# Kernel optimization log

Measured on AMD Instinct MI355X. Metric: run time of the kernel, lower is better.

The kernel has to match this reference:

```python
import jax, jax.numpy as jnp
import numpy as np

S, B, H, K = 2048, 64, 8, 12          # seq_len, input_bits, num_heads, bits per RAM neuron
N_POS = 11                             # bits for relative distance in [0, max_seq_len-1]


def setup_inputs() -> dict:
    key = jax.random.key(0)
    k1, k2, k3, k4, k5 = jax.random.split(key, 5)
    tokens = jax.random.randint(k1, (S, B), 0, 2, dtype=jnp.int32)            # bit tokens
    conn_heads = jax.random.randint(k2, (H, K), 0, 2 * B + N_POS, dtype=jnp.int32)
    head_table = jnp.round(jax.random.uniform(k3, (H, 1 << K))).astype(jnp.float32)  # {0,1} RAM cells
    conn_v = jax.random.randint(k4, (B, K), 0, B, dtype=jnp.int32)
    table_v = jnp.round(jax.random.uniform(k5, (B, 1 << K))).astype(jnp.float32)     # {0,1} RAM cells
    return {"tokens": tokens, "conn_heads": conn_heads, "head_table": head_table,
            "conn_v": conn_v, "table_v": table_v}


def reference(tokens, conn_heads, head_table, conn_v, table_v):
    pow2 = (1 << (K - 1 - jnp.arange(K))).astype(jnp.int32)                 # [K] MSB-first
    tok = tokens.astype(jnp.int32)                                           # [S,B]

    # split each head's 12 connections into query / key / relative-position groups
    grp_q = (conn_heads < B).astype(jnp.int32)
    grp_k = ((conn_heads >= B) & (conn_heads < 2 * B)).astype(jnp.int32)
    grp_p = (conn_heads >= 2 * B).astype(jnp.int32)
    cq = jnp.clip(conn_heads, 0, B - 1)
    ck = jnp.clip(conn_heads - B, 0, B - 1)
    cp = jnp.clip(conn_heads - 2 * B, 0, N_POS - 1)

    # additive address decomposition: addr(i,j,h) = addr_q(i,h)+addr_k(j,h)+addr_p(i-j,h)
    addr_q = (tok[:, cq] * (grp_q * pow2)[None]).sum(-1)                     # [S,H]
    addr_k = (tok[:, ck] * (grp_k * pow2)[None]).sum(-1)                     # [S,H]
    ar = jnp.arange(S)
    posb = ((ar[:, None] >> (N_POS - 1 - jnp.arange(N_POS))[None, :]) & 1).astype(jnp.int32)  # [S,N_POS]
    addr_p = (posb[:, cp] * (grp_p * pow2)[None]).sum(-1)                    # [S,H] indexed by rel dist

    rel = jnp.clip(ar[:, None] - ar[None, :], 0)                             # [S,S]
    addr = addr_q[:, None, :] + addr_k[None, :, :] + addr_p[rel]             # [S,S,H]

    # per-head table lookup, sum over heads = vote counts
    votes = head_table[jnp.arange(H)[None, None, :], addr].sum(-1)           # [S,S]
    causal = ar[None, :] <= ar[:, None]
    votes = jnp.where(causal, votes, 0.0)

    # bit-level value projection: one RAM neuron per output bit
    addr_v = (tok[:, conn_v] * pow2[None, None, :]).sum(-1)                  # [S,B]
    values = table_v[jnp.arange(B)[None, :], addr_v]                         # [S,B]

    # TOP_1 aggregation: first key with max vote; zeros if max vote is 0
    max_vote = votes.max(axis=1)                                             # [S]
    best = jnp.argmax(votes, axis=1)                                         # first occurrence, like the loop
    out = jnp.where((max_vote > 0)[:, None], values[best], 0.0)              # [S,B]
    return out
```

## Files before the change

kernel.cpp:

```cpp
#include <hip/hip_runtime.h>


#define SS 2048
#define BB 64
#define HH 8
#define KK 12
#define NPOS 11
#define TBL 4096
#define TBLW (TBL / 32)

typedef unsigned short u16;
typedef unsigned int u32;
typedef unsigned long long u64;

#define SEG_A (SS * HH)
#define SEG_B (HH * TBL)
#define SEG_C (SS * BB)
#define TOTAL (SEG_A + SEG_B + SEG_C)

__global__ __launch_bounds__(256) void precompute_kernel(
    const int* __restrict__ tokens,
    const int* __restrict__ conn_heads,
    const float* __restrict__ head_table,
    const int* __restrict__ conn_v,
    u16* __restrict__ A16, u16* __restrict__ AK16, u16* __restrict__ P16,
    u32* __restrict__ bits, u16* __restrict__ V16)
{
    const int gid = blockIdx.x * 256 + threadIdx.x;
    if (gid < SEG_A) {
        const int s = gid >> 3;
        const int h = gid & 7;
        int aq = 0, ak = 0, ap = 0;
        #pragma unroll
        for (int k = 0; k < KK; ++k) {
            const int c = conn_heads[h * KK + k];
            const int sh = KK - 1 - k;
            const int cq = min(c, BB - 1);
            const int ck = min(max(c - BB, 0), BB - 1);
            const int cp = min(max(c - 2 * BB, 0), NPOS - 1);
            const int tq = tokens[s * BB + cq] & 1;
            const int tk = tokens[s * BB + ck] & 1;
            const int tp = (s >> (NPOS - 1 - cp)) & 1;
            aq |= (c < BB ? tq : 0) << sh;
            ap |= (c >= 2 * BB ? tp : 0) << sh;
            ak |= ((c >= BB) && (c < 2 * BB) ? tk : 0) << sh;
        }
        A16[gid]  = (u16)aq;
        AK16[gid] = (u16)ak;
        P16[gid]  = (u16)ap;
    } else if (gid < SEG_A + SEG_B) {
        const int t = gid - SEG_A;
        const u64 m = __ballot(head_table[t] > 0.5f);
        if ((t & 63) == 0) {
            bits[(t >> 5) + 0] = (u32)m;
            bits[(t >> 5) + 1] = (u32)(m >> 32);
        }
    } else {
        const int t = gid - (SEG_A + SEG_B);
        const int s = t >> 6;
        const int b = t & 63;
        int av = 0;
        #pragma unroll
        for (int k = 0; k < KK; ++k) {
            av |= (tokens[s * BB + conn_v[b * KK + k]] & 1) << (KK - 1 - k);
        }
        V16[t] = (u16)av;
    }
}

__device__ __forceinline__ int votes_packed(const u32* sbits,
                                            const uint4& q, const uint4& kk, const uint4& pp)
{
    int v = 0;
    u32 w, a0, a1;
    w = q.x | kk.x | pp.x;
    a0 = w & 0xFFFFu; a1 = w >> 16;
    v += (sbits[0 * TBLW + (a0 >> 5)] >> (a0 & 31)) & 1;
    v += (sbits[1 * TBLW + (a1 >> 5)] >> (a1 & 31)) & 1;
    w = q.y | kk.y | pp.y;
    a0 = w & 0xFFFFu; a1 = w >> 16;
    v += (sbits[2 * TBLW + (a0 >> 5)] >> (a0 & 31)) & 1;
    v += (sbits[3 * TBLW + (a1 >> 5)] >> (a1 & 31)) & 1;
    w = q.z | kk.z | pp.z;
    a0 = w & 0xFFFFu; a1 = w >> 16;
    v += (sbits[4 * TBLW + (a0 >> 5)] >> (a0 & 31)) & 1;
    v += (sbits[5 * TBLW + (a1 >> 5)] >> (a1 & 31)) & 1;
    w = q.w | kk.w | pp.w;
    a0 = w & 0xFFFFu; a1 = w >> 16;
    v += (sbits[6 * TBLW + (a0 >> 5)] >> (a0 & 31)) & 1;
    v += (sbits[7 * TBLW + (a1 >> 5)] >> (a1 & 31)) & 1;
    return v;
}

__global__ __launch_bounds__(256, 4) void vote_kernel(
    const u16* __restrict__ A16, const u16* __restrict__ AK16, const u16* __restrict__ P16,
    const u32* __restrict__ bits_g,
    const u16* __restrict__ V16,
    const float* __restrict__ table_v,
    float* __restrict__ out)
{
    __shared__ u32 sbits[HH * TBLW];
    __shared__ u32 skey[2][4];

    const int tid = threadIdx.x;
    const int b = blockIdx.x;
    const int i0 = b;
    const int i1 = SS - 1 - b;

    ((uint4*)sbits)[tid] = ((const uint4*)bits_g)[tid];
    __syncthreads();

    const uint4 q0 = *(const uint4*)(A16 + i0 * HH);
    const uint4 q1 = *(const uint4*)(A16 + i1 * HH);

    u32 key0 = 0u, key1 = 0u;

    uint4 kkv[8], ppv[8];
    #pragma unroll
    for (int it = 0; it < 8; ++it) {
        const int c = (it << 8) + tid;
        const bool r0 = (c <= i0);
        const int j = r0 ? c : (c - i0 - 1);
        const int d = r0 ? (i0 - c) : (2048 - c);
        kkv[it] = *(const uint4*)(AK16 + j * HH);
        ppv[it] = *(const uint4*)(P16 + d * HH);
    }
    #pragma unroll
    for (int it = 0; it < 8; ++it) {
        const int c = (it << 8) + tid;
        const bool r0 = (c <= i0);
        const int j = r0 ? c : (c - i0 - 1);
        const uint4 q = r0 ? q0 : q1;
        const int v = votes_packed(sbits, q, kkv[it], ppv[it]);
        const u32 key = ((u32)v << 12) | (u32)(4095 - j);
        if (r0) { key0 = key0 > key ? key0 : key; }
        else    { key1 = key1 > key ? key1 : key; }
    }
    if (tid == 0) {
        const uint4 kk = *(const uint4*)(AK16 + i1 * HH);
        const uint4 pp = *(const uint4*)(P16);
        const int v = votes_packed(sbits, q1, kk, pp);
        const u32 key = ((u32)v << 12) | (u32)(4095 - i1);
        key1 = key1 > key ? key1 : key;
    }

    #pragma unroll
    for (int off = 32; off > 0; off >>= 1) {
        u32 o0 = (u32)__shfl_xor((int)key0, off, 64);
        u32 o1 = (u32)__shfl_xor((int)key1, off, 64);
        key0 = key0 > o0 ? key0 : o0;
        key1 = key1 > o1 ? key1 : o1;
    }
    if ((tid & 63) == 0) {
        skey[0][tid >> 6] = key0;
        skey[1][tid >> 6] = key1;
    }
    __syncthreads();

    if (tid < 128) {
        const int r = tid >> 6;
        const int lane = tid & 63;
        u32 ka = skey[r][0] > skey[r][1] ? skey[r][0] : skey[r][1];
        u32 kb = skey[r][2] > skey[r][3] ? skey[r][2] : skey[r][3];
        u32 kf = ka > kb ? ka : kb;
        const int row = r ? i1 : i0;
        float o = 0.0f;
        if ((kf >> 12) > 0) {
            const int best = 4095 - (int)(kf & 4095u);
            o = table_v[lane * TBL + (int)V16[best * BB + lane]];
        }
        out[row * BB + lane] = o;
    }
}

extern "C" void kernel_launch(void* const* d_in, const int* in_sizes, int n_in,
                              void* d_out, int out_size, void* d_ws, size_t ws_size,
                              hipStream_t stream) {
    const int*   tokens     = (const int*)d_in[0];
    const int*   conn_heads = (const int*)d_in[1];
    const float* head_table = (const float*)d_in[2];
    const int*   conn_v     = (const int*)d_in[3];
    const float* table_v    = (const float*)d_in[4];
    float* out = (float*)d_out;

    char* w = (char*)d_ws;
    u16* A16  = (u16*)(w);
    u16* AK16 = (u16*)(w + 32768);
    u16* P16  = (u16*)(w + 65536);
    u32* bits = (u32*)(w + 98304);
    u16* V16  = (u16*)(w + 102400);

    precompute_kernel<<<TOTAL / 256, 256, 0, stream>>>(
        tokens, conn_heads, head_table, conn_v, A16, AK16, P16, bits, V16);
    vote_kernel<<<SS / 2, 256, 0, stream>>>(
        A16, AK16, P16, bits, V16, table_v, out);
}
```

Before: 70.89 us.

## Replicate head bit tables 8x in LDS to cut bank conflicts, async-load via global_load_lds

The precompute kernel now writes each 32-bit word of the packed head tables eight times, interleaved so that copy c sits in a different LDS bank. Each vote thread reads copy (tid&7), which spreads random table lookups across more banks and reduces conflicts. The LDS fill now uses global_load_lds direct-to-LDS loads issued before the key/position loads, with the barrier moved after them so the copies overlap. LDS use grows from 4KB to 32KB per block, which may cap occupancy, and the replicated table makes more global traffic per block.

```diff
diff --git a/kernel.cpp b/kernel.cpp
--- a/kernel.cpp
+++ b/kernel.cpp
@@ -8,6 +8,8 @@
 #define NPOS 11
 #define TBL 4096
 #define TBLW (TBL / 32)
+#define NREP 8
+#define HREPW (TBLW * NREP)
 
 typedef unsigned short u16;
 typedef unsigned int u32;
@@ -24,7 +26,7 @@
     const float* __restrict__ head_table,
     const int* __restrict__ conn_v,
     u16* __restrict__ A16, u16* __restrict__ AK16, u16* __restrict__ P16,
-    u32* __restrict__ bits, u16* __restrict__ V16)
+    u32* __restrict__ bits_rep, u16* __restrict__ V16)
 {
     const int gid = blockIdx.x * 256 + threadIdx.x;
     if (gid < SEG_A) {
@@ -51,9 +53,14 @@
     } else if (gid < SEG_A + SEG_B) {
         const int t = gid - SEG_A;
         const u64 m = __ballot(head_table[t] > 0.5f);
-        if ((t & 63) == 0) {
-            bits[(t >> 5) + 0] = (u32)m;
-            bits[(t >> 5) + 1] = (u32)(m >> 32);
+        if ((t & 31) == 0) {
+            const u32 wv = (t & 32) ? (u32)(m >> 32) : (u32)m;
+            const int h = t >> 12;
+            const int wl = (t & (TBL - 1)) >> 5;
+            #pragma unroll
+            for (int c = 0; c < NREP; ++c) {
+                bits_rep[h * HREPW + wl * NREP + c] = wv;
+            }
         }
     } else {
         const int t = gid - (SEG_A + SEG_B);
@@ -68,52 +75,63 @@
     }
 }
 
-__device__ __forceinline__ int votes_packed(const u32* sbits,
+__device__ __forceinline__ int votes_packed(const u32* sbits, const int crep,
                                             const uint4& q, const uint4& kk, const uint4& pp)
 {
     int v = 0;
     u32 w, a0, a1;
     w = q.x | kk.x | pp.x;
     a0 = w & 0xFFFFu; a1 = w >> 16;
-    v += (sbits[0 * TBLW + (a0 >> 5)] >> (a0 & 31)) & 1;
-    v += (sbits[1 * TBLW + (a1 >> 5)] >> (a1 & 31)) & 1;
+    v += (sbits[0 * HREPW + ((a0 >> 5) << 3) + crep] >> (a0 & 31)) & 1;
+    v += (sbits[1 * HREPW + ((a1 >> 5) << 3) + crep] >> (a1 & 31)) & 1;
     w = q.y | kk.y | pp.y;
     a0 = w & 0xFFFFu; a1 = w >> 16;
-    v += (sbits[2 * TBLW + (a0 >> 5)] >> (a0 & 31)) & 1;
-    v += (sbits[3 * TBLW + (a1 >> 5)] >> (a1 & 31)) & 1;
+    v += (sbits[2 * HREPW + ((a0 >> 5) << 3) + crep] >> (a0 & 31)) & 1;
+    v += (sbits[3 * HREPW + ((a1 >> 5) << 3) + crep] >> (a1 & 31)) & 1;
     w = q.z | kk.z | pp.z;
     a0 = w & 0xFFFFu; a1 = w >> 16;
-    v += (sbits[4 * TBLW + (a0 >> 5)] >> (a0 & 31)) & 1;
-    v += (sbits[5 * TBLW + (a1 >> 5)] >> (a1 & 31)) & 1;
+    v += (sbits[4 * HREPW + ((a0 >> 5) << 3) + crep] >> (a0 & 31)) & 1;
+    v += (sbits[5 * HREPW + ((a1 >> 5) << 3) + crep] >> (a1 & 31)) & 1;
     w = q.w | kk.w | pp.w;
     a0 = w & 0xFFFFu; a1 = w >> 16;
-    v += (sbits[6 * TBLW + (a0 >> 5)] >> (a0 & 31)) & 1;
-    v += (sbits[7 * TBLW + (a1 >> 5)] >> (a1 & 31)) & 1;
+    v += (sbits[6 * HREPW + ((a0 >> 5) << 3) + crep] >> (a0 & 31)) & 1;
+    v += (sbits[7 * HREPW + ((a1 >> 5) << 3) + crep] >> (a1 & 31)) & 1;
     return v;
 }
 
 __global__ __launch_bounds__(256, 4) void vote_kernel(
     const u16* __restrict__ A16, const u16* __restrict__ AK16, const u16* __restrict__ P16,
-    const u32* __restrict__ bits_g,
+    const u32* __restrict__ bits_rep,
     const u16* __restrict__ V16,
     const float* __restrict__ table_v,
     float* __restrict__ out)
 {
-    __shared__ u32 sbits[HH * TBLW];
+    __shared__ u32 sbits[HH * HREPW];
     __shared__ u32 skey[2][4];
 
     const int tid = threadIdx.x;
+    const int crep = tid & 7;
     const int b = blockIdx.x;
     const int i0 = b;
     const int i1 = SS - 1 - b;
 
-    ((uint4*)sbits)[tid] = ((const uint4*)bits_g)[tid];
-    __syncthreads();
+    {
+        const int wv = tid >> 6;
+        const int ln = tid & 63;
+        #pragma unroll
+        for (int r = 0; r < 8; ++r) {
+            const int byteoff = (wv * 8 + r) << 10;
+            __builtin_amdgcn_global_load_lds(
+                (const __attribute__((address_space(1))) unsigned int*)
+                    ((const char*)bits_rep + byteoff + ln * 16),
+                (__attribute__((address_space(3))) unsigned int*)
+                    ((char*)sbits + byteoff),
+                16, 0, 0);
+        }
+    }
 
     const uint4 q0 = *(const uint4*)(A16 + i0 * HH);
     const uint4 q1 = *(const uint4*)(A16 + i1 * HH);
-
-    u32 key0 = 0u, key1 = 0u;
 
     uint4 kkv[8], ppv[8];
     #pragma unroll
@@ -125,13 +143,17 @@
         kkv[it] = *(const uint4*)(AK16 + j * HH);
         ppv[it] = *(const uint4*)(P16 + d * HH);
     }
+    __syncthreads();
+
+    u32 key0 = 0u, key1 = 0u;
+
     #pragma unroll
     for (int it = 0; it < 8; ++it) {
         const int c = (it << 8) + tid;
         const bool r0 = (c <= i0);
         const int j = r0 ? c : (c - i0 - 1);
         const uint4 q = r0 ? q0 : q1;
-        const int v = votes_packed(sbits, q, kkv[it], ppv[it]);
+        const int v = votes_packed(sbits, crep, q, kkv[it], ppv[it]);
         const u32 key = ((u32)v << 12) | (u32)(4095 - j);
         if (r0) { key0 = key0 > key ? key0 : key; }
         else    { key1 = key1 > key ? key1 : key; }
@@ -139,7 +161,7 @@
     if (tid == 0) {
         const uint4 kk = *(const uint4*)(AK16 + i1 * HH);
         const uint4 pp = *(const uint4*)(P16);
-        const int v = votes_packed(sbits, q1, kk, pp);
+        const int v = votes_packed(sbits, 0, q1, kk, pp);
         const u32 key = ((u32)v << 12) | (u32)(4095 - i1);
         key1 = key1 > key ? key1 : key;
     }
@@ -184,14 +206,14 @@
     float* out = (float*)d_out;
 
     char* w = (char*)d_ws;
-    u16* A16  = (u16*)(w);
-    u16* AK16 = (u16*)(w + 32768);
-    u16* P16  = (u16*)(w + 65536);
-    u32* bits = (u32*)(w + 98304);
-    u16* V16  = (u16*)(w + 102400);
+    u16* A16      = (u16*)(w);
+    u16* AK16     = (u16*)(w + 32768);
+    u16* P16      = (u16*)(w + 65536);
+    u32* bits_rep = (u32*)(w + 98304);
+    u16* V16      = (u16*)(w + 131072);
 
     precompute_kernel<<<TOTAL / 256, 256, 0, stream>>>(
-        tokens, conn_heads, head_table, conn_v, A16, AK16, P16, bits, V16);
+        tokens, conn_heads, head_table, conn_v, A16, AK16, P16, bits_rep, V16);
     vote_kernel<<<SS / 2, 256, 0, stream>>>(
-        A16, AK16, P16, bits, V16, table_v, out);
-}
+        A16, AK16, P16, bits_rep, V16, table_v, out);
+}
```

After: 72.56 us. +2.4%, slower.
